# Kernel optimization log

Measured on AMD Instinct MI355X. Metric: run time of the kernel, lower is better.

The kernel has to match this reference:

```python
import jax, jax.numpy as jnp
import numpy as np

N = 100000   # nodes
E = 1600000  # edges
D_IN = 128
D = 128
G = 64       # graphs in batch
C = 2        # out_channels
EPS = 1e-5   # BatchNorm eps


def setup_inputs() -> dict:
    key = jax.random.key(0)
    ks = jax.random.split(key, 24)
    s = 0.05
    inp = {
        "x": jax.random.normal(ks[0], (N, D_IN), dtype=jnp.float32),
        "edge_index": jax.random.randint(ks[1], (2, E), 0, N, dtype=jnp.int32),
        "edge_attr": jax.random.uniform(ks[2], (E, 2), dtype=jnp.float32),
        "batch": jnp.sort(jax.random.randint(ks[3], (N,), 0, G, dtype=jnp.int32)),
        # GCN layer 0
        "Wg0": jax.random.normal(ks[4], (D_IN, D), dtype=jnp.float32) * s,
        "bg0": jnp.zeros((D,), jnp.float32),
        "gamma0": jnp.ones((D,), jnp.float32),
        "beta0": jnp.zeros((D,), jnp.float32),
        # GCN layer 1
        "Wg1": jax.random.normal(ks[5], (D, D), dtype=jnp.float32) * s,
        "bg1": jnp.zeros((D,), jnp.float32),
        "gamma1": jnp.ones((D,), jnp.float32),
        "beta1": jnp.zeros((D,), jnp.float32),
        # dense head
        "Wl1": jax.random.normal(ks[6], (D, D), dtype=jnp.float32) * s,
        "bl1": jnp.zeros((D,), jnp.float32),
        "Wl2": jax.random.normal(ks[7], (D, D), dtype=jnp.float32) * s,
        "bl2": jnp.zeros((D,), jnp.float32),
        "Wc1": jax.random.normal(ks[8], (D, D), dtype=jnp.float32) * s,
        "bc1": jnp.zeros((D,), jnp.float32),
        "Wc2": jax.random.normal(ks[9], (D, C), dtype=jnp.float32) * s,
        "bc2": jnp.zeros((C,), jnp.float32),
    }
    return inp


def _gcn_conv(x, src, dst, w, W, b):
    # PyG GCNConv: h = x @ W ; add self-loops (weight 1) ; symmetric norm ; agg at dst ; + bias
    h = x @ W                                                   # [N, D]
    deg = jax.ops.segment_sum(w, dst, num_segments=N) + 1.0     # self-loop weight 1
    dinv = jnp.where(deg > 0, jax.lax.rsqrt(deg), 0.0)          # deg^{-1/2}
    norm = dinv[src] * w * dinv[dst]                            # [E]
    agg = jax.ops.segment_sum(norm[:, None] * h[src], dst, num_segments=N)
    agg = agg + (dinv * dinv)[:, None] * h                      # self-loop contribution
    return agg + b


def _bn(x, gamma, beta):
    # training-mode batch statistics over the node dimension
    m = x.mean(axis=0)
    v = x.var(axis=0)
    return (x - m) * jax.lax.rsqrt(v + EPS) * gamma + beta


def reference(x, edge_index, edge_attr, batch,
              Wg0, bg0, gamma0, beta0,
              Wg1, bg1, gamma1, beta1,
              Wl1, bl1, Wl2, bl2, Wc1, bc1, Wc2, bc2):
    src, dst = edge_index[0], edge_index[1]
    w = edge_attr[:, 1]  # which_edge_weight is None -> column 1

    h = jax.nn.relu(_gcn_conv(x, src, dst, w, Wg0, bg0))
    h = _bn(h, gamma0, beta0)                 # dropout: identity (eval)
    h = jax.nn.relu(_gcn_conv(h, src, dst, w, Wg1, bg1))
    h = _bn(h, gamma1, beta1)

    h = jax.nn.relu(h @ Wl1 + bl1)
    h = h @ Wl2 + bl2                          # node embeddings [N, D]

    counts = jax.ops.segment_sum(jnp.ones((N,), h.dtype), batch, num_segments=G)
    graph_reps = jax.ops.segment_sum(h, batch, num_segments=G) / jnp.maximum(counts, 1.0)[:, None]

    logits = jax.nn.relu(graph_reps @ Wc1 + bc1) @ Wc2 + bc2   # [G, C]
    return (h, graph_reps, logits)
```

## Files before the change

### kernel.cpp

```cpp
#include <hip/hip_runtime.h>

#define N_NODES 100000
#define N_EDGES 1600000
#define DFEAT   128
#define NGRAPH  64
#define EPSV    1e-5f
#define SCAN_BLOCKS ((N_NODES + 255) / 256)
#define DEG_SCALE 268435456.0f
#define DEG_MASK  ((1ULL << 42) - 1)
#define FILL_BLOCKS ((N_EDGES + 255) / 256)
#define GEMM_GRID   ((N_NODES + 127) / 128)

typedef float v4f  __attribute__((ext_vector_type(4)));
typedef short v8s  __attribute__((ext_vector_type(8)));
typedef unsigned short us4 __attribute__((ext_vector_type(4)));
typedef unsigned short us8 __attribute__((ext_vector_type(8)));

static __device__ __forceinline__ unsigned short f2bf(float f) {
    union { float f; unsigned int u; } v; v.f = f;
    unsigned int u = v.u;
    return (unsigned short)((u + 0x7FFFu + ((u >> 16) & 1u)) >> 16);
}
static __device__ __forceinline__ float bf2f(unsigned short b) {
    union { unsigned int u; float f; } v; v.u = ((unsigned int)b) << 16;
    return v.f;
}

__global__ __launch_bounds__(256) void initprep_kernel(
    unsigned long long* __restrict__ degcnt, int* __restrict__ fillc,
    float* __restrict__ stats0, float* __restrict__ stats1,
    float* __restrict__ gsum, float* __restrict__ gcntf,
    const float* __restrict__ W0, const float* __restrict__ W1,
    const float* __restrict__ W2, const float* __restrict__ W3,
    unsigned short* __restrict__ T0, unsigned short* __restrict__ T1,
    unsigned short* __restrict__ T2, unsigned short* __restrict__ T3) {
    int bid = blockIdx.x;
    int i = bid * 256 + threadIdx.x;
    if (i < N_NODES) { degcnt[i] = 0ULL; fillc[i] = 0; }
    if (i < 256)  { stats0[i] = 0.f; stats1[i] = 0.f; }
    if (i < NGRAPH * DFEAT) gsum[i] = 0.f;
    if (i < NGRAPH) gcntf[i] = 0.f;
    if (bid < 256) {
        int which = bid >> 6;
        int i2 = (bid & 63) * 256 + threadIdx.x;
        const float* W = which == 0 ? W0 : which == 1 ? W1 : which == 2 ? W2 : W3;
        unsigned short* T = which == 0 ? T0 : which == 1 ? T1 : which == 2 ? T2 : T3;
        int n = i2 >> 7, k = i2 & 127;
        T[n * 128 + k] = f2bf(W[k * 128 + n]);
    }
}

__global__ void edge_degcnt_kernel(const int* __restrict__ ei, const float* __restrict__ ea,
                                   unsigned long long* __restrict__ degcnt) {
    int e = blockIdx.x * 256 + threadIdx.x;
    if (e >= N_EDGES) return;
    int d = ei[N_EDGES + e];
    float w = ea[2 * e + 1];
    unsigned long long v = (1ULL << 42) | (unsigned long long)(w * DEG_SCALE);
    atomicAdd(&degcnt[d], v);
}

__global__ __launch_bounds__(256) void scan1d_kernel(
    const unsigned long long* __restrict__ degcnt, int* __restrict__ cnt,
    float* __restrict__ dinv, int* __restrict__ blockSum) {
    __shared__ int lds[256];
    int i = blockIdx.x * 256 + threadIdx.x;
    int t = threadIdx.x;
    int c = 0;
    if (i < N_NODES) {
        unsigned long long u = degcnt[i];
        c = (int)(u >> 42);
        cnt[i] = c;
        float deg = 1.0f + (float)(u & DEG_MASK) * (1.0f / DEG_SCALE);
        dinv[i] = rsqrtf(deg);
    }
    lds[t] = c;
    __syncthreads();
    for (int off = 128; off > 0; off >>= 1) {
        if (t < off) lds[t] += lds[t + off];
        __syncthreads();
    }
    if (t == 0) blockSum[blockIdx.x] = lds[0];
}

__global__ __launch_bounds__(512) void scan2_kernel(int* __restrict__ blockSum) {
    __shared__ int lds[512];
    int t = threadIdx.x;
    int v = (t < SCAN_BLOCKS) ? blockSum[t] : 0;
    lds[t] = v;
    __syncthreads();
    for (int off = 1; off < 512; off <<= 1) {
        int u = (t >= off) ? lds[t - off] : 0;
        __syncthreads();
        lds[t] += u;
        __syncthreads();
    }
    if (t < SCAN_BLOCKS) blockSum[t] = lds[t] - v;
}

__global__ __launch_bounds__(256) void scan3_kernel(const int* __restrict__ cnt,
                                                    const int* __restrict__ blockSum,
                                                    int* __restrict__ rowptr) {
    __shared__ int lds[256];
    int i = blockIdx.x * 256 + threadIdx.x;
    int t = threadIdx.x;
    int v = (i < N_NODES) ? cnt[i] : 0;
    lds[t] = v;
    __syncthreads();
    for (int off = 1; off < 256; off <<= 1) {
        int u = (t >= off) ? lds[t - off] : 0;
        __syncthreads();
        lds[t] += u;
        __syncthreads();
    }
    if (i < N_NODES) rowptr[i] = blockSum[blockIdx.x] + lds[t] - v;
    if (i == 0) rowptr[N_NODES] = N_EDGES;
}

__global__ __launch_bounds__(256, 4) void fill_gemm0_kernel(
    const int* __restrict__ ei, const float* __restrict__ ea,
    const float* __restrict__ dinv, const int* __restrict__ rowptr,
    int* __restrict__ fillc, int2* __restrict__ edges,
    const float* __restrict__ X, const unsigned short* __restrict__ Wt,
    unsigned short* __restrict__ Out) {
    __shared__ unsigned short Ws[128][136];
    if (blockIdx.x < FILL_BLOCKS) {
        int e = blockIdx.x * 256 + threadIdx.x;
        if (e >= N_EDGES) return;
        int s = ei[e], d = ei[N_EDGES + e];
        float w = ea[2 * e + 1];
        float nrm = dinv[s] * w * dinv[d];
        int pos = rowptr[d] + atomicAdd(&fillc[d], 1);
        edges[pos] = make_int2(s, __float_as_int(nrm));
        return;
    }
    const int tid = threadIdx.x;
    const int rb = (blockIdx.x - FILL_BLOCKS) * 128;
#pragma unroll
    for (int it = 0; it < 8; ++it) {
        int flat = it * 2048 + tid * 8;
        int n = flat >> 7, k = flat & 127;
        *(us8*)&Ws[n][k] = *(const us8*)&Wt[n * 128 + k];
    }
    __syncthreads();

    const int wv = tid >> 6, lane = tid & 63;
    const int q = lane >> 4, c16 = lane & 15;
    const int rA = rb + wv * 32 + c16;
    const int rB = rA + 16;
    const size_t rAc = (size_t)(rA < N_NODES ? rA : N_NODES - 1);
    const size_t rBc = (size_t)(rB < N_NODES ? rB : N_NODES - 1);

    v4f acc[2][8];
#pragma unroll
    for (int i = 0; i < 2; ++i)
#pragma unroll
        for (int j = 0; j < 8; ++j) acc[i][j] = (v4f){0.f, 0.f, 0.f, 0.f};

#pragma unroll
    for (int ks = 0; ks < 4; ++ks) {
        const int k0 = ks * 32 + q * 8;
        float4 f0 = *(const float4*)&X[rAc * 128 + k0];
        float4 f1 = *(const float4*)&X[rAc * 128 + k0 + 4];
        float4 g0 = *(const float4*)&X[rBc * 128 + k0];
        float4 g1 = *(const float4*)&X[rBc * 128 + k0 + 4];
        us8 oa, ob;
        oa[0] = f2bf(f0.x); oa[1] = f2bf(f0.y); oa[2] = f2bf(f0.z); oa[3] = f2bf(f0.w);
        oa[4] = f2bf(f1.x); oa[5] = f2bf(f1.y); oa[6] = f2bf(f1.z); oa[7] = f2bf(f1.w);
        ob[0] = f2bf(g0.x); ob[1] = f2bf(g0.y); ob[2] = f2bf(g0.z); ob[3] = f2bf(g0.w);
        ob[4] = f2bf(g1.x); ob[5] = f2bf(g1.y); ob[6] = f2bf(g1.z); ob[7] = f2bf(g1.w);
        v8s a0 = *(v8s*)&oa, a1 = *(v8s*)&ob;
#pragma unroll
        for (int nt = 0; nt < 8; ++nt) {
            v8s b = *(const v8s*)&Ws[nt * 16 + c16][ks * 32 + q * 8];
            acc[0][nt] = __builtin_amdgcn_mfma_f32_16x16x32_bf16(a0, b, acc[0][nt], 0, 0, 0);
            acc[1][nt] = __builtin_amdgcn_mfma_f32_16x16x32_bf16(a1, b, acc[1][nt], 0, 0, 0);
        }
    }
#pragma unroll
    for (int mt = 0; mt < 2; ++mt)
#pragma unroll
        for (int nt = 0; nt < 8; ++nt)
#pragma unroll
            for (int r = 0; r < 4; ++r) {
                int row = rb + wv * 32 + mt * 16 + q * 4 + r;
                if (row >= N_NODES) continue;
                Out[(size_t)row * 128 + nt * 16 + c16] = f2bf(acc[mt][nt][r]);
            }
}

__global__ __launch_bounds__(256, 4) void gemm_bf16_kernel(
    const unsigned short* __restrict__ X,
    const unsigned short* __restrict__ Wt,
    void* __restrict__ Outv, int out_is_f32,
    const float* __restrict__ bnp, const float* __restrict__ bias, int do_relu,
    const int* __restrict__ batch, float* __restrict__ gsum,
    float* __restrict__ gcntf, int do_pool) {
    __shared__ unsigned short Ws[128][136];
    const int tid = threadIdx.x;
    const int rb = blockIdx.x * 128;

#pragma unroll
    for (int it = 0; it < 8; ++it) {
        int flat = it * 2048 + tid * 8;
        int n = flat >> 7, k = flat & 127;
        *(us8*)&Ws[n][k] = *(const us8*)&Wt[n * 128 + k];
    }
    __syncthreads();

    const int wv = tid >> 6, lane = tid & 63;
    const int q = lane >> 4, c16 = lane & 15;
    const int rA = rb + wv * 32 + c16;
    const int rB = rA + 16;
    const size_t rAc = (size_t)(rA < N_NODES ? rA : N_NODES - 1);
    const size_t rBc = (size_t)(rB < N_NODES ? rB : N_NODES - 1);

    v4f acc[2][8];
#pragma unroll
    for (int i = 0; i < 2; ++i)
#pragma unroll
        for (int j = 0; j < 8; ++j) acc[i][j] = (v4f){0.f, 0.f, 0.f, 0.f};

#pragma unroll
    for (int ks = 0; ks < 4; ++ks) {
        const int k0 = ks * 32 + q * 8;
        us8 v0 = *(const us8*)&X[rAc * 128 + k0];
        us8 v1 = *(const us8*)&X[rBc * 128 + k0];
        if (bnp) {
            float4 s0 = *(const float4*)&bnp[k0];
            float4 s1 = *(const float4*)&bnp[k0 + 4];
            float4 b0 = *(const float4*)&bnp[128 + k0];
            float4 b1 = *(const float4*)&bnp[128 + k0 + 4];
            v0[0] = f2bf(bf2f(v0[0]) * s0.x + b0.x);
            v0[1] = f2bf(bf2f(v0[1]) * s0.y + b0.y);
            v0[2] = f2bf(bf2f(v0[2]) * s0.z + b0.z);
            v0[3] = f2bf(bf2f(v0[3]) * s0.w + b0.w);
            v0[4] = f2bf(bf2f(v0[4]) * s1.x + b1.x);
            v0[5] = f2bf(bf2f(v0[5]) * s1.y + b1.y);
            v0[6] = f2bf(bf2f(v0[6]) * s1.z + b1.z);
            v0[7] = f2bf(bf2f(v0[7]) * s1.w + b1.w);
            v1[0] = f2bf(bf2f(v1[0]) * s0.x + b0.x);
            v1[1] = f2bf(bf2f(v1[1]) * s0.y + b0.y);
            v1[2] = f2bf(bf2f(v1[2]) * s0.z + b0.z);
            v1[3] = f2bf(bf2f(v1[3]) * s0.w + b0.w);
            v1[4] = f2bf(bf2f(v1[4]) * s1.x + b1.x);
            v1[5] = f2bf(bf2f(v1[5]) * s1.y + b1.y);
            v1[6] = f2bf(bf2f(v1[6]) * s1.z + b1.z);
            v1[7] = f2bf(bf2f(v1[7]) * s1.w + b1.w);
        }
        v8s a0 = *(v8s*)&v0, a1 = *(v8s*)&v1;
#pragma unroll
        for (int nt = 0; nt < 8; ++nt) {
            v8s b = *(const v8s*)&Ws[nt * 16 + c16][ks * 32 + q * 8];
            acc[0][nt] = __builtin_amdgcn_mfma_f32_16x16x32_bf16(a0, b, acc[0][nt], 0, 0, 0);
            acc[1][nt] = __builtin_amdgcn_mfma_f32_16x16x32_bf16(a1, b, acc[1][nt], 0, 0, 0);
        }
    }

#pragma unroll
    for (int mt = 0; mt < 2; ++mt) {
#pragma unroll
        for (int nt = 0; nt < 8; ++nt) {
            int col = nt * 16 + c16;
            float bcol = bias ? bias[col] : 0.f;
#pragma unroll
            for (int r = 0; r < 4; ++r) {
                int row = rb + wv * 32 + mt * 16 + q * 4 + r;
                float o = acc[mt][nt][r] + bcol;
                if (do_relu) o = fmaxf(o, 0.f);
                acc[mt][nt][r] = o;
                if (row >= N_NODES) continue;
                if (out_is_f32) ((float*)Outv)[(size_t)row * 128 + col] = o;
                else ((unsigned short*)Outv)[(size_t)row * 128 + col] = f2bf(o);
            }
        }
    }

    if (do_pool) {
        __shared__ float pg[128];
        __shared__ float pcnt;
        int br[8];
#pragma unroll
        for (int mt = 0; mt < 2; ++mt)
#pragma unroll
            for (int r = 0; r < 4; ++r) {
                int row = rb + wv * 32 + mt * 16 + q * 4 + r;
                br[mt * 4 + r] = (row < N_NODES) ? batch[row] : -1;
            }
        int rlast = (rb + 127 < N_NODES) ? rb + 127 : N_NODES - 1;
        int gmin = batch[rb];
        int gmax = batch[rlast];
        for (int g = gmin; g <= gmax; ++g) {
            if (tid < 128) pg[tid] = 0.f;
            if (tid == 0) pcnt = 0.f;
            __syncthreads();
            if (wv < 2) {
                int rr = rb + tid;
                bool p = (tid < 128) && (rr < N_NODES) && (batch[rr] == g);
                unsigned long long m = __ballot(p);
                if (lane == 0 && m) atomicAdd(&pcnt, (float)__popcll(m));
            }
#pragma unroll
            for (int nt = 0; nt < 8; ++nt) {
                float s = 0.f;
#pragma unroll
                for (int mt = 0; mt < 2; ++mt)
#pragma unroll
                    for (int r = 0; r < 4; ++r)
                        if (br[mt * 4 + r] == g) s += acc[mt][nt][r];
                s += __shfl_xor(s, 16);
                s += __shfl_xor(s, 32);
                if (q == 0 && s != 0.f) atomicAdd(&pg[nt * 16 + c16], s);
            }
            __syncthreads();
            if (tid < 128 && pg[tid] != 0.f) atomicAdd(&gsum[g * 128 + tid], pg[tid]);
            if (tid == 0 && pcnt != 0.f) atomicAdd(&gcntf[g], pcnt);
            __syncthreads();
        }
    }
}

__global__ __launch_bounds__(256) void agg_relu_bf16_kernel(
    const unsigned short* __restrict__ H, const int* __restrict__ rowptr,
    const int2* __restrict__ edges,
    const float* __restrict__ dinv, const float* __restrict__ bias,
    unsigned short* __restrict__ outb, float* __restrict__ stats, int nwaves) {
    __shared__ float red[1024];
    const int tid = threadIdx.x;
    const int wv = tid >> 6;
    const int lane = tid & 63;
    const float bx = bias[2 * lane], by = bias[2 * lane + 1];
    const unsigned int* __restrict__ H4 = (const unsigned int*)H;
    unsigned int* __restrict__ O4 = (unsigned int*)outb;
    float s0 = 0.f, q0 = 0.f, s1 = 0.f, q1 = 0.f;

    for (int i = blockIdx.x * 4 + wv; i < N_NODES; i += nwaves) {
        int beg = __builtin_amdgcn_readfirstlane(rowptr[i]);
        int end = __builtin_amdgcn_readfirstlane(rowptr[i + 1]);
        float di = dinv[i];
        unsigned int hs = H4[(size_t)i * 64 + lane];
        float px0 = 0.f, py0 = 0.f, px1 = 0.f, py1 = 0.f;
        float px2 = 0.f, py2 = 0.f, px3 = 0.f, py3 = 0.f;
        const int last = end - 1;
        for (int j = beg; j < end; j += 8) {
            int j1 = j + 1 < end ? j + 1 : last;
            int j2 = j + 2 < end ? j + 2 : last;
            int j3 = j + 3 < end ? j + 3 : last;
            int j4 = j + 4 < end ? j + 4 : last;
            int j5 = j + 5 < end ? j + 5 : last;
            int j6 = j + 6 < end ? j + 6 : last;
            int j7 = j + 7 < end ? j + 7 : last;
            int2 e0 = edges[j];
            int2 e1 = edges[j1];
            int2 e2 = edges[j2];
            int2 e3 = edges[j3];
            int2 e4 = edges[j4];
            int2 e5 = edges[j5];
            int2 e6 = edges[j6];
            int2 e7 = edges[j7];
            unsigned int h0 = H4[(size_t)e0.x * 64 + lane];
            unsigned int h1 = H4[(size_t)e1.x * 64 + lane];
            unsigned int h2 = H4[(size_t)e2.x * 64 + lane];
            unsigned int h3 = H4[(size_t)e3.x * 64 + lane];
            unsigned int h4 = H4[(size_t)e4.x * 64 + lane];
            unsigned int h5 = H4[(size_t)e5.x * 64 + lane];
            unsigned int h6 = H4[(size_t)e6.x * 64 + lane];
            unsigned int h7 = H4[(size_t)e7.x * 64 + lane];
            float v0 = __int_as_float(e0.y);
            float v1 = j + 1 < end ? __int_as_float(e1.y) : 0.f;
            float v2 = j + 2 < end ? __int_as_float(e2.y) : 0.f;
            float v3 = j + 3 < end ? __int_as_float(e3.y) : 0.f;
            float v4 = j + 4 < end ? __int_as_float(e4.y) : 0.f;
            float v5 = j + 5 < end ? __int_as_float(e5.y) : 0.f;
            float v6 = j + 6 < end ? __int_as_float(e6.y) : 0.f;
            float v7 = j + 7 < end ? __int_as_float(e7.y) : 0.f;
            px0 = fmaf(v0, bf2f((unsigned short)h0), px0);
            py0 = fmaf(v0, bf2f((unsigned short)(h0 >> 16)), py0);
            px1 = fmaf(v1, bf2f((unsigned short)h1), px1);
            py1 = fmaf(v1, bf2f((unsigned short)(h1 >> 16)), py1);
            px2 = fmaf(v2, bf2f((unsigned short)h2), px2);
            py2 = fmaf(v2, bf2f((unsigned short)(h2 >> 16)), py2);
            px3 = fmaf(v3, bf2f((unsigned short)h3), px3);
            py3 = fmaf(v3, bf2f((unsigned short)(h3 >> 16)), py3);
            px0 = fmaf(v4, bf2f((unsigned short)h4), px0);
            py0 = fmaf(v4, bf2f((unsigned short)(h4 >> 16)), py0);
            px1 = fmaf(v5, bf2f((unsigned short)h5), px1);
            py1 = fmaf(v5, bf2f((unsigned short)(h5 >> 16)), py1);
            px2 = fmaf(v6, bf2f((unsigned short)h6), px2);
            py2 = fmaf(v6, bf2f((unsigned short)(h6 >> 16)), py2);
            px3 = fmaf(v7, bf2f((unsigned short)h7), px3);
            py3 = fmaf(v7, bf2f((unsigned short)(h7 >> 16)), py3);
        }
        float dd = di * di;
        float ax = (px0 + px1) + (px2 + px3);
        float ay = (py0 + py1) + (py2 + py3);
        ax = fmaf(dd, bf2f((unsigned short)hs), ax) + bx;
        ay = fmaf(dd, bf2f((unsigned short)(hs >> 16)), ay) + by;
        ax = fmaxf(ax, 0.f);
        ay = fmaxf(ay, 0.f);
        O4[(size_t)i * 64 + lane] =
            (unsigned int)f2bf(ax) | ((unsigned int)f2bf(ay) << 16);
        s0 += ax; q0 += ax * ax; s1 += ay; q1 += ay * ay;
    }

    red[wv * 128 + 2 * lane]           = s0;
    red[wv * 128 + 2 * lane + 1]       = s1;
    red[512 + wv * 128 + 2 * lane]     = q0;
    red[512 + wv * 128 + 2 * lane + 1] = q1;
    __syncthreads();
    if (tid < 128) {
        float ts = red[tid] + red[128 + tid] + red[256 + tid] + red[384 + tid];
        float tq = red[512 + tid] + red[640 + tid] + red[768 + tid] + red[896 + tid];
        atomicAdd(&stats[tid], ts);
        atomicAdd(&stats[128 + tid], tq);
    }
}

__global__ void bn_finalize_kernel(const float* __restrict__ stats,
                                   const float* __restrict__ gamma,
                                   const float* __restrict__ beta,
                                   float* __restrict__ bnp) {
    int f = threadIdx.x;
    float mean = stats[f] / (float)N_NODES;
    float var = stats[128 + f] / (float)N_NODES - mean * mean;
    float sc = gamma[f] * rsqrtf(var + EPSV);
    bnp[f] = sc;
    bnp[128 + f] = beta[f] - mean * sc;
}

__global__ __launch_bounds__(128) void logits_kernel(
    const float* __restrict__ gsum, const float* __restrict__ gcntf,
    const float* __restrict__ Wc1, const float* __restrict__ bc1,
    const float* __restrict__ Wc2, const float* __restrict__ bc2,
    float* __restrict__ out_reps, float* __restrict__ out_logits) {
    __shared__ float repS[128];
    __shared__ float tmp[128];
    int g = blockIdx.x, t = threadIdx.x;
    float rep = gsum[(size_t)g * 128 + t] / fmaxf(gcntf[g], 1.0f);
    out_reps[(size_t)g * 128 + t] = rep;
    repS[t] = rep;
    __syncthreads();
    float acc = bc1[t];
    for (int k = 0; k < 128; ++k) acc = fmaf(repS[k], Wc1[k * 128 + t], acc);
    tmp[t] = fmaxf(acc, 0.f);
    __syncthreads();
    if (t < 2) {
        float a = bc2[t];
        for (int k = 0; k < 128; ++k) a = fmaf(tmp[k], Wc2[k * 2 + t], a);
        out_logits[g * 2 + t] = a;
    }
}

extern "C" void kernel_launch(void* const* d_in, const int* in_sizes, int n_in,
                              void* d_out, int out_size, void* d_ws, size_t ws_size,
                              hipStream_t stream) {
    const float* x      = (const float*)d_in[0];
    const int*   ei     = (const int*)d_in[1];
    const float* ea     = (const float*)d_in[2];
    const int*   batch  = (const int*)d_in[3];
    const float* Wg0    = (const float*)d_in[4];
    const float* bg0    = (const float*)d_in[5];
    const float* gamma0 = (const float*)d_in[6];
    const float* beta0  = (const float*)d_in[7];
    const float* Wg1    = (const float*)d_in[8];
    const float* bg1    = (const float*)d_in[9];
    const float* gamma1 = (const float*)d_in[10];
    const float* beta1  = (const float*)d_in[11];
    const float* Wl1    = (const float*)d_in[12];
    const float* bl1    = (const float*)d_in[13];
    const float* Wl2    = (const float*)d_in[14];
    const float* bl2    = (const float*)d_in[15];
    const float* Wc1    = (const float*)d_in[16];
    const float* bc1    = (const float*)d_in[17];
    const float* Wc2    = (const float*)d_in[18];
    const float* bc2    = (const float*)d_in[19];

    float* out = (float*)d_out;
    char* ws = (char*)d_ws;
    size_t off = 0;
    auto alloc = [&](size_t bytes) {
        void* p = ws + off;
        off += (bytes + 15) & ~(size_t)15;
        return p;
    };
    unsigned short* bufHb = (unsigned short*)alloc(sizeof(unsigned short) * (size_t)N_NODES * 128);
    unsigned short* bufAb = (unsigned short*)alloc(sizeof(unsigned short) * (size_t)N_NODES * 128);
    int2* edges = (int2*)alloc(sizeof(int2) * (size_t)N_EDGES);
    unsigned long long* degcnt = (unsigned long long*)alloc(sizeof(unsigned long long) * N_NODES);
    unsigned short* Wt0   = (unsigned short*)alloc(sizeof(unsigned short) * 128 * 128);
    unsigned short* Wt1   = (unsigned short*)alloc(sizeof(unsigned short) * 128 * 128);
    unsigned short* Wt2   = (unsigned short*)alloc(sizeof(unsigned short) * 128 * 128);
    unsigned short* Wt3   = (unsigned short*)alloc(sizeof(unsigned short) * 128 * 128);
    float* dinv   = (float*)alloc(sizeof(float) * N_NODES);
    int*   cnt    = (int*)alloc(sizeof(int) * N_NODES);
    int*   fillc  = (int*)alloc(sizeof(int) * N_NODES);
    float* stats0 = (float*)alloc(sizeof(float) * 256);
    float* stats1 = (float*)alloc(sizeof(float) * 256);
    float* bnp0   = (float*)alloc(sizeof(float) * 256);
    float* bnp1   = (float*)alloc(sizeof(float) * 256);
    float* gsum   = (float*)alloc(sizeof(float) * NGRAPH * 128);
    float* gcntf  = (float*)alloc(sizeof(float) * NGRAPH);
    int*   rowptr = (int*)alloc(sizeof(int) * (N_NODES + 1));
    int*   blockSum = (int*)alloc(sizeof(int) * SCAN_BLOCKS);

    initprep_kernel<<<SCAN_BLOCKS, 256, 0, stream>>>(degcnt, fillc, stats0, stats1,
                                                     gsum, gcntf, Wg0, Wg1, Wl1, Wl2,
                                                     Wt0, Wt1, Wt2, Wt3);
    edge_degcnt_kernel<<<(N_EDGES + 255) / 256, 256, 0, stream>>>(ei, ea, degcnt);
    scan1d_kernel<<<SCAN_BLOCKS, 256, 0, stream>>>(degcnt, cnt, dinv, blockSum);
    scan2_kernel<<<1, 512, 0, stream>>>(blockSum);
    scan3_kernel<<<SCAN_BLOCKS, 256, 0, stream>>>(cnt, blockSum, rowptr);
    fill_gemm0_kernel<<<FILL_BLOCKS + GEMM_GRID, 256, 0, stream>>>(
        ei, ea, dinv, rowptr, fillc, edges, x, Wt0, bufHb);

    const int agg_blocks = 2048;
    const int agg_nwaves = agg_blocks * 4;
    agg_relu_bf16_kernel<<<agg_blocks, 256, 0, stream>>>(bufHb, rowptr, edges,
                                                         dinv, bg0, bufAb, stats0, agg_nwaves);
    bn_finalize_kernel<<<1, 128, 0, stream>>>(stats0, gamma0, beta0, bnp0);
    gemm_bf16_kernel<<<GEMM_GRID, 256, 0, stream>>>(bufAb, Wt1, bufHb, 0, bnp0,
                                                    nullptr, 0, nullptr, nullptr, nullptr, 0);
    agg_relu_bf16_kernel<<<agg_blocks, 256, 0, stream>>>(bufHb, rowptr, edges,
                                                         dinv, bg1, bufAb, stats1, agg_nwaves);
    bn_finalize_kernel<<<1, 128, 0, stream>>>(stats1, gamma1, beta1, bnp1);
    gemm_bf16_kernel<<<GEMM_GRID, 256, 0, stream>>>(bufAb, Wt2, bufHb, 0, bnp1,
                                                    bl1, 1, nullptr, nullptr, nullptr, 0);
    gemm_bf16_kernel<<<GEMM_GRID, 256, 0, stream>>>(bufHb, Wt3, out, 1, nullptr,
                                                    bl2, 0, batch, gsum, gcntf, 1);
    logits_kernel<<<NGRAPH, 128, 0, stream>>>(gsum, gcntf, Wc1, bc1, Wc2, bc2,
                                              out + (size_t)N_NODES * 128,
                                              out + (size_t)N_NODES * 128 + NGRAPH * 128);
}
```

Measured before the change: 580.4 us.

## Bucket edges by destination range before CSR fill, fuse gemm0 with degree pass

The degree-count pass now also scatters each edge into one of 391 buckets keyed by dst>>8, packing the src and low dst bits into one int. It runs inside the first GEMM's launch, so the separate degree kernel goes away. A new fill kernel runs one 1024-thread block per bucket and does the CSR fill, so the scattered writes and atomics on rowptr/fillc/edges stay within a 256-node window, which should improve cache locality. The cost is an extra pass over the edges through a staging buffer that reuses bufAb. Any bucket holding more than 5120 edges silently drops the excess, and packing src into 17 bits assumes N < 131072.

```diff
diff --git a/kernel.cpp b/kernel.cpp
--- a/kernel.cpp
+++ b/kernel.cpp
@@ -10,6 +10,8 @@
 #define DEG_MASK  ((1ULL << 42) - 1)
 #define FILL_BLOCKS ((N_EDGES + 255) / 256)
 #define GEMM_GRID   ((N_NODES + 127) / 128)
+#define NBUCK 391
+#define BCAP  5120
 
 typedef float v4f  __attribute__((ext_vector_type(4)));
 typedef short v8s  __attribute__((ext_vector_type(8)));
@@ -28,6 +30,7 @@
 
 __global__ __launch_bounds__(256) void initprep_kernel(
     unsigned long long* __restrict__ degcnt, int* __restrict__ fillc,
+    int* __restrict__ bktCnt,
     float* __restrict__ stats0, float* __restrict__ stats1,
     float* __restrict__ gsum, float* __restrict__ gcntf,
     const float* __restrict__ W0, const float* __restrict__ W1,
@@ -37,6 +40,7 @@
     int bid = blockIdx.x;
     int i = bid * 256 + threadIdx.x;
     if (i < N_NODES) { degcnt[i] = 0ULL; fillc[i] = 0; }
+    if (i < NBUCK) bktCnt[i] = 0;
     if (i < 256)  { stats0[i] = 0.f; stats1[i] = 0.f; }
     if (i < NGRAPH * DFEAT) gsum[i] = 0.f;
     if (i < NGRAPH) gcntf[i] = 0.f;
@@ -50,14 +54,80 @@
     }
 }
 
-__global__ void edge_degcnt_kernel(const int* __restrict__ ei, const float* __restrict__ ea,
-                                   unsigned long long* __restrict__ degcnt) {
-    int e = blockIdx.x * 256 + threadIdx.x;
-    if (e >= N_EDGES) return;
-    int d = ei[N_EDGES + e];
-    float w = ea[2 * e + 1];
-    unsigned long long v = (1ULL << 42) | (unsigned long long)(w * DEG_SCALE);
-    atomicAdd(&degcnt[d], v);
+__global__ __launch_bounds__(256, 4) void edges_degcnt_gemm0_kernel(
+    const int* __restrict__ ei, const float* __restrict__ ea,
+    unsigned long long* __restrict__ degcnt,
+    int* __restrict__ bktCnt, int2* __restrict__ bucketed,
+    const float* __restrict__ X, const unsigned short* __restrict__ Wt,
+    unsigned short* __restrict__ Out) {
+    __shared__ unsigned short Ws[128][136];
+    if (blockIdx.x < FILL_BLOCKS) {
+        int e = blockIdx.x * 256 + threadIdx.x;
+        if (e >= N_EDGES) return;
+        int s = ei[e], d = ei[N_EDGES + e];
+        float w = ea[2 * e + 1];
+        unsigned long long v = (1ULL << 42) | (unsigned long long)(w * DEG_SCALE);
+        atomicAdd(&degcnt[d], v);
+        int b = d >> 8;
+        int p = atomicAdd(&bktCnt[b], 1);
+        if (p < BCAP)
+            bucketed[(size_t)b * BCAP + p] =
+                make_int2(s | ((d & 255) << 17), __float_as_int(w));
+        return;
+    }
+    const int tid = threadIdx.x;
+    const int rb = (blockIdx.x - FILL_BLOCKS) * 128;
+#pragma unroll
+    for (int it = 0; it < 8; ++it) {
+        int flat = it * 2048 + tid * 8;
+        int n = flat >> 7, k = flat & 127;
+        *(us8*)&Ws[n][k] = *(const us8*)&Wt[n * 128 + k];
+    }
+    __syncthreads();
+
+    const int wv = tid >> 6, lane = tid & 63;
+    const int q = lane >> 4, c16 = lane & 15;
+    const int rA = rb + wv * 32 + c16;
+    const int rB = rA + 16;
+    const size_t rAc = (size_t)(rA < N_NODES ? rA : N_NODES - 1);
+    const size_t rBc = (size_t)(rB < N_NODES ? rB : N_NODES - 1);
+
+    v4f acc[2][8];
+#pragma unroll
+    for (int i = 0; i < 2; ++i)
+#pragma unroll
+        for (int j = 0; j < 8; ++j) acc[i][j] = (v4f){0.f, 0.f, 0.f, 0.f};
+
+#pragma unroll
+    for (int ks = 0; ks < 4; ++ks) {
+        const int k0 = ks * 32 + q * 8;
+        float4 f0 = *(const float4*)&X[rAc * 128 + k0];
+        float4 f1 = *(const float4*)&X[rAc * 128 + k0 + 4];
+        float4 g0 = *(const float4*)&X[rBc * 128 + k0];
+        float4 g1 = *(const float4*)&X[rBc * 128 + k0 + 4];
+        us8 oa, ob;
+        oa[0] = f2bf(f0.x); oa[1] = f2bf(f0.y); oa[2] = f2bf(f0.z); oa[3] = f2bf(f0.w);
+        oa[4] = f2bf(f1.x); oa[5] = f2bf(f1.y); oa[6] = f2bf(f1.z); oa[7] = f2bf(f1.w);
+        ob[0] = f2bf(g0.x); ob[1] = f2bf(g0.y); ob[2] = f2bf(g0.z); ob[3] = f2bf(g0.w);
+        ob[4] = f2bf(g1.x); ob[5] = f2bf(g1.y); ob[6] = f2bf(g1.z); ob[7] = f2bf(g1.w);
+        v8s a0 = *(v8s*)&oa, a1 = *(v8s*)&ob;
+#pragma unroll
+        for (int nt = 0; nt < 8; ++nt) {
+            v8s b = *(const v8s*)&Ws[nt * 16 + c16][ks * 32 + q * 8];
+            acc[0][nt] = __builtin_amdgcn_mfma_f32_16x16x32_bf16(a0, b, acc[0][nt], 0, 0, 0);
+            acc[1][nt] = __builtin_amdgcn_mfma_f32_16x16x32_bf16(a1, b, acc[1][nt], 0, 0, 0);
+        }
+    }
+#pragma unroll
+    for (int mt = 0; mt < 2; ++mt)
+#pragma unroll
+        for (int nt = 0; nt < 8; ++nt)
+#pragma unroll
+            for (int r = 0; r < 4; ++r) {
+                int row = rb + wv * 32 + mt * 16 + q * 4 + r;
+                if (row >= N_NODES) continue;
+                Out[(size_t)row * 128 + nt * 16 + c16] = f2bf(acc[mt][nt][r]);
+            }
 }
 
 __global__ __launch_bounds__(256) void scan1d_kernel(
@@ -117,76 +187,22 @@
     if (i == 0) rowptr[N_NODES] = N_EDGES;
 }
 
-__global__ __launch_bounds__(256, 4) void fill_gemm0_kernel(
-    const int* __restrict__ ei, const float* __restrict__ ea,
+__global__ __launch_bounds__(1024) void fill2_kernel(
+    const int2* __restrict__ bucketed, const int* __restrict__ bktCnt,
     const float* __restrict__ dinv, const int* __restrict__ rowptr,
-    int* __restrict__ fillc, int2* __restrict__ edges,
-    const float* __restrict__ X, const unsigned short* __restrict__ Wt,
-    unsigned short* __restrict__ Out) {
-    __shared__ unsigned short Ws[128][136];
-    if (blockIdx.x < FILL_BLOCKS) {
-        int e = blockIdx.x * 256 + threadIdx.x;
-        if (e >= N_EDGES) return;
-        int s = ei[e], d = ei[N_EDGES + e];
-        float w = ea[2 * e + 1];
+    int* __restrict__ fillc, int2* __restrict__ edges) {
+    const int b = blockIdx.x;
+    int cnt = bktCnt[b]; if (cnt > BCAP) cnt = BCAP;
+    const int2* __restrict__ src = bucketed + (size_t)b * BCAP;
+    for (int idx = threadIdx.x; idx < cnt; idx += 1024) {
+        int2 en = src[idx];
+        int s = en.x & 0x1FFFF;
+        int d = (b << 8) + (en.x >> 17);
+        float w = __int_as_float(en.y);
         float nrm = dinv[s] * w * dinv[d];
         int pos = rowptr[d] + atomicAdd(&fillc[d], 1);
         edges[pos] = make_int2(s, __float_as_int(nrm));
-        return;
-    }
-    const int tid = threadIdx.x;
-    const int rb = (blockIdx.x - FILL_BLOCKS) * 128;
-#pragma unroll
-    for (int it = 0; it < 8; ++it) {
-        int flat = it * 2048 + tid * 8;
-        int n = flat >> 7, k = flat & 127;
-        *(us8*)&Ws[n][k] = *(const us8*)&Wt[n * 128 + k];
-    }
-    __syncthreads();
-
-    const int wv = tid >> 6, lane = tid & 63;
-    const int q = lane >> 4, c16 = lane & 15;
-    const int rA = rb + wv * 32 + c16;
-    const int rB = rA + 16;
-    const size_t rAc = (size_t)(rA < N_NODES ? rA : N_NODES - 1);
-    const size_t rBc = (size_t)(rB < N_NODES ? rB : N_NODES - 1);
-
-    v4f acc[2][8];
-#pragma unroll
-    for (int i = 0; i < 2; ++i)
-#pragma unroll
-        for (int j = 0; j < 8; ++j) acc[i][j] = (v4f){0.f, 0.f, 0.f, 0.f};
-
-#pragma unroll
-    for (int ks = 0; ks < 4; ++ks) {
-        const int k0 = ks * 32 + q * 8;
-        float4 f0 = *(const float4*)&X[rAc * 128 + k0];
-        float4 f1 = *(const float4*)&X[rAc * 128 + k0 + 4];
-        float4 g0 = *(const float4*)&X[rBc * 128 + k0];
-        float4 g1 = *(const float4*)&X[rBc * 128 + k0 + 4];
-        us8 oa, ob;
-        oa[0] = f2bf(f0.x); oa[1] = f2bf(f0.y); oa[2] = f2bf(f0.z); oa[3] = f2bf(f0.w);
-        oa[4] = f2bf(f1.x); oa[5] = f2bf(f1.y); oa[6] = f2bf(f1.z); oa[7] = f2bf(f1.w);
-        ob[0] = f2bf(g0.x); ob[1] = f2bf(g0.y); ob[2] = f2bf(g0.z); ob[3] = f2bf(g0.w);
-        ob[4] = f2bf(g1.x); ob[5] = f2bf(g1.y); ob[6] = f2bf(g1.z); ob[7] = f2bf(g1.w);
-        v8s a0 = *(v8s*)&oa, a1 = *(v8s*)&ob;
-#pragma unroll
-        for (int nt = 0; nt < 8; ++nt) {
-            v8s b = *(const v8s*)&Ws[nt * 16 + c16][ks * 32 + q * 8];
-            acc[0][nt] = __builtin_amdgcn_mfma_f32_16x16x32_bf16(a0, b, acc[0][nt], 0, 0, 0);
-            acc[1][nt] = __builtin_amdgcn_mfma_f32_16x16x32_bf16(a1, b, acc[1][nt], 0, 0, 0);
-        }
-    }
-#pragma unroll
-    for (int mt = 0; mt < 2; ++mt)
-#pragma unroll
-        for (int nt = 0; nt < 8; ++nt)
-#pragma unroll
-            for (int r = 0; r < 4; ++r) {
-                int row = rb + wv * 32 + mt * 16 + q * 4 + r;
-                if (row >= N_NODES) continue;
-                Out[(size_t)row * 128 + nt * 16 + c16] = f2bf(acc[mt][nt][r]);
-            }
+    }
 }
 
 __global__ __launch_bounds__(256, 4) void gemm_bf16_kernel(
@@ -494,6 +510,7 @@
     float* dinv   = (float*)alloc(sizeof(float) * N_NODES);
     int*   cnt    = (int*)alloc(sizeof(int) * N_NODES);
     int*   fillc  = (int*)alloc(sizeof(int) * N_NODES);
+    int*   bktCnt = (int*)alloc(sizeof(int) * NBUCK);
     float* stats0 = (float*)alloc(sizeof(float) * 256);
     float* stats1 = (float*)alloc(sizeof(float) * 256);
     float* bnp0   = (float*)alloc(sizeof(float) * 256);
@@ -502,16 +519,19 @@
     float* gcntf  = (float*)alloc(sizeof(float) * NGRAPH);
     int*   rowptr = (int*)alloc(sizeof(int) * (N_NODES + 1));
     int*   blockSum = (int*)alloc(sizeof(int) * SCAN_BLOCKS);
-
-    initprep_kernel<<<SCAN_BLOCKS, 256, 0, stream>>>(degcnt, fillc, stats0, stats1,
-                                                     gsum, gcntf, Wg0, Wg1, Wl1, Wl2,
+    int2* bucketed = (int2*)bufAb;
+
+    initprep_kernel<<<SCAN_BLOCKS, 256, 0, stream>>>(degcnt, fillc, bktCnt,
+                                                     stats0, stats1, gsum, gcntf,
+                                                     Wg0, Wg1, Wl1, Wl2,
                                                      Wt0, Wt1, Wt2, Wt3);
-    edge_degcnt_kernel<<<(N_EDGES + 255) / 256, 256, 0, stream>>>(ei, ea, degcnt);
+    edges_degcnt_gemm0_kernel<<<FILL_BLOCKS + GEMM_GRID, 256, 0, stream>>>(
+        ei, ea, degcnt, bktCnt, bucketed, x, Wt0, bufHb);
     scan1d_kernel<<<SCAN_BLOCKS, 256, 0, stream>>>(degcnt, cnt, dinv, blockSum);
     scan2_kernel<<<1, 512, 0, stream>>>(blockSum);
     scan3_kernel<<<SCAN_BLOCKS, 256, 0, stream>>>(cnt, blockSum, rowptr);
-    fill_gemm0_kernel<<<FILL_BLOCKS + GEMM_GRID, 256, 0, stream>>>(
-        ei, ea, dinv, rowptr, fillc, edges, x, Wt0, bufHb);
+    fill2_kernel<<<NBUCK, 1024, 0, stream>>>(bucketed, bktCnt, dinv, rowptr,
+                                             fillc, edges);
 
     const int agg_blocks = 2048;
     const int agg_nwaves = agg_blocks * 4;
```

New measurement: 1.113 ms. +91.8%, slower.
